# Kernel optimization log

Hardware: AMD Instinct MI355X
Metric: run time of the kernel (lower is better)

Reference implementation:

```python
import jax, jax.numpy as jnp
import numpy as np

# --- CQT configuration derived from the layer's __init__ defaults ---
SR = 44100
N_OCTAVES = 7
BINS_PER_SEMITONE = 3
BPO = BINS_PER_SEMITONE * 12            # 36 bins per octave
N_BINS = BPO * N_OCTAVES                # 252 bins
HOP = (int(SR * 11 / 1000.0) // 4) * 4  # 485 -> 484 (hop - hop % 4)
FMIN = 32.70319566257483                # librosa default fmin = C1
Q = 1.0 / (2.0 ** (1.0 / BPO) - 1.0)    # constant-Q factor, filter_scale=1

_FREQS = FMIN * 2.0 ** (np.arange(N_BINS) / BPO)   # [252] center freqs
_LENGTHS = Q * SR / _FREQS                         # per-bin window lengths
MAX_LEN = int(np.ceil(_LENGTHS[0]))                # longest kernel (lowest bin)
CENTER = MAX_LEN // 2
SIG_LEN = 220500                                   # 5 s of audio
N_FRAMES = 1 + SIG_LEN // HOP                      # 456 (centered framing)


def _cqt_kernels():
    """Complex CQT kernel bank, returned as (real, imag) of shape [N_BINS, MAX_LEN].
    Each bin uses a Hann window of its own constant-Q length, centered in MAX_LEN,
    modulated at its center frequency; L1-normalized window and 1/sqrt(L) scaling
    (matching librosa's norm=1 filters with scale=True)."""
    t = jnp.arange(MAX_LEN, dtype=jnp.float32) - CENTER          # centered time axis
    freqs = jnp.asarray(_FREQS, dtype=jnp.float32)[:, None]      # [252, 1]
    L = jnp.asarray(_LENGTHS, dtype=jnp.float32)[:, None]        # [252, 1]
    two_pi = 2.0 * np.pi
    # Hann window of length L_i centered at t=0, zero outside |t| < L_i/2
    win = jnp.where(jnp.abs(t)[None, :] < L / 2,
                    0.5 * (1.0 + jnp.cos(two_pi * t[None, :] / L)),
                    0.0)
    ang = two_pi * freqs * t[None, :] / SR
    norm = win.sum(axis=-1, keepdims=True) * jnp.sqrt(L)
    kr = win * jnp.cos(ang) / norm
    ki = win * jnp.sin(ang) / norm
    return kr, ki


def setup_inputs() -> dict:
    key = jax.random.key(0)
    signal = jax.random.normal(key, (SIG_LEN,), dtype=jnp.float32)
    return {"signal": signal}


def reference(signal) -> jnp.ndarray:
    kr, ki = _cqt_kernels()                                      # [252, MAX_LEN] each
    padded = jnp.pad(signal, (CENTER, CENTER))                   # center=True framing
    idx = (jnp.arange(N_FRAMES)[:, None] * HOP
           + jnp.arange(MAX_LEN)[None, :])                       # [456, MAX_LEN]
    frames = padded[idx]                                         # [456, MAX_LEN]
    cr = frames @ kr.T                                           # [456, 252] real part
    ci = frames @ ki.T                                           # [456, 252] imag part
    mag = jnp.sqrt(cr * cr + ci * ci)                            # |CQT|
    return mag.T                                                 # [252, 456] = (n_bins, n_frames)
```

## Files before the change

kernel.cpp:

```cpp
#include <hip/hip_runtime.h>
#include <hip/hip_bf16.h>
#include <math.h>

#define NBINS    252
#define NFRAMES  456
#define HOPSZ    484
#define SIGLEN   220500
#define PADOFF   34688
#define XBF_ELEMS 317440
#define SRD      44100.0
#define FMIND    32.70319566257483
#define TWO_PI_D 6.283185307179586476925287
#define MAXCH    288
#define SC       32
#define CHUNK_BYTES (SC*2048)
#define CHUNK_ELEMS (SC*1024)

typedef unsigned short ushort_t;
typedef __attribute__((ext_vector_type(8))) short bf16x8;
typedef __attribute__((ext_vector_type(4))) float f32x4;

struct ChunkTab { int2 e[MAXCH]; };

__global__ __launch_bounds__(256) void pad_bf16(const float* __restrict__ sig,
                                                ushort_t* __restrict__ xbf) {
  int i = blockIdx.x * 256 + threadIdx.x;
  if (i < XBF_ELEMS) {
    int s = i - PADOFF;
    float v = (s >= 0 && s < SIGLEN) ? sig[s] : 0.0f;
    __hip_bfloat16 h = __float2bfloat16(v);
    xbf[i] = *reinterpret_cast<ushort_t*>(&h);
  }
}

__global__ __launch_bounds__(256) void norm_kernel(float* __restrict__ nrm) {
  int b = blockIdx.x * 256 + threadIdx.x;
  if (b >= NBINS) return;
  const double PI = 3.14159265358979323846;
  double freq = FMIND * exp2((double)b / 36.0);
  double Q = 1.0 / (exp2(1.0 / 36.0) - 1.0);
  double L = Q * SRD / freq;
  int T = (int)(L * 0.5);
  double N = (double)(2 * T + 1);
  double win_sum = 0.5 * N - 0.5 * (sin(PI * (N - L) / L) / sin(PI / L));
  nrm[b] = (float)(1.0 / (win_sum * sqrt(L)));
}

__global__ __launch_bounds__(256) void gen_bank(ushort_t* __restrict__ bank, ChunkTab tab) {
  int c = blockIdx.y;
  int e = blockIdx.x * 256 + threadIdx.x;
  int ks = e >> 7;
  int rem = e & 127;
  int frag = (rem >> 6) & 1;
  int lane = rem & 63;
  int bl = lane & 15, kb = lane >> 4;
  int g = tab.e[c].x, jadj = tab.e[c].y;
  int b = g * 16 + bl;
  int t0 = jadj + ks * 32 + kb * 8;

  ushort_t res[8];
#pragma unroll
  for (int j = 0; j < 8; ++j) res[j] = 0;

  if (b < NBINS) {
    double freq = FMIND * exp2((double)b / 36.0);
    double fos = freq / SRD;
    double Q = 1.0 / (exp2(1.0 / 36.0) - 1.0);
    double L = Q * SRD / freq;
    int T = (int)(L * 0.5);
    if (t0 + 7 >= -T && t0 <= T) {
      double rv = fos * (double)t0; rv -= floor(rv);
      float ang0 = (float)(rv * TWO_PI_D);
      float dang = (float)(fos * TWO_PI_D);
      float invL = (float)(1.0 / L);
#pragma unroll
      for (int j = 0; j < 8; ++j) {
        int tt = t0 + j;
        if (tt >= -T && tt <= T) {
          float win = 0.5f + 0.5f * __cosf(6.2831853f * ((float)tt * invL));
          float s, cc;
          __sincosf(ang0 + (float)j * dang, &s, &cc);
          float val = win * (frag ? s : cc);
          __hip_bfloat16 h = __float2bfloat16(val);
          res[j] = *reinterpret_cast<ushort_t*>(&h);
        }
      }
    }
  }
  union { ushort_t u[8]; uint4 v; } pk;
#pragma unroll
  for (int j = 0; j < 8; ++j) pk.u[j] = res[j];
  *reinterpret_cast<uint4*>(bank + (size_t)c * CHUNK_ELEMS + ks * 1024 + frag * 512 + lane * 8) = pk.v;
}

__global__ __launch_bounds__(256) void zero_accum(float* __restrict__ acc) {
  acc[blockIdx.x * 256 + threadIdx.x] = 0.0f;
}

__global__ __launch_bounds__(256) void cqt_mfma(const ushort_t* __restrict__ xbf,
                                                const ushort_t* __restrict__ bank,
                                                float* __restrict__ accum,
                                                ChunkTab tab) {
  const int tid = threadIdx.x;
  const int lane = tid & 63;
  const int w = tid >> 6;
  const int c = blockIdx.y;
  const int g = tab.e[c].x, jadj = tab.e[c].y;
  const int bl = lane & 15, kb = lane >> 4;
  const int fbase = blockIdx.x * 128 + w * 32;

  const ushort_t* pA0 = xbf + (PADOFF + (fbase + bl) * HOPSZ + jadj + kb * 8);
  const ushort_t* pA1 = pA0 + 16 * HOPSZ;
  const ushort_t* pB  = bank + (size_t)c * CHUNK_ELEMS + lane * 8;

  f32x4 ar0 = {0.f, 0.f, 0.f, 0.f};
  f32x4 ai0 = ar0, ar1 = ar0, ai1 = ar0;

#pragma unroll 4
  for (int ks = 0; ks < SC; ++ks) {
    union { uint2 q[2]; bf16x8 v; } a0, a1;
    a0.q[0] = *reinterpret_cast<const uint2*>(pA0 + ks * 32);
    a0.q[1] = *reinterpret_cast<const uint2*>(pA0 + ks * 32 + 4);
    a1.q[0] = *reinterpret_cast<const uint2*>(pA1 + ks * 32);
    a1.q[1] = *reinterpret_cast<const uint2*>(pA1 + ks * 32 + 4);
    union { uint4 q; bf16x8 v; } bk, bi;
    bk.q = *reinterpret_cast<const uint4*>(pB + ks * 1024);
    bi.q = *reinterpret_cast<const uint4*>(pB + ks * 1024 + 512);
    ar0 = __builtin_amdgcn_mfma_f32_16x16x32_bf16(a0.v, bk.v, ar0, 0, 0, 0);
    ai0 = __builtin_amdgcn_mfma_f32_16x16x32_bf16(a0.v, bi.v, ai0, 0, 0, 0);
    ar1 = __builtin_amdgcn_mfma_f32_16x16x32_bf16(a1.v, bk.v, ar1, 0, 0, 0);
    ai1 = __builtin_amdgcn_mfma_f32_16x16x32_bf16(a1.v, bi.v, ai1, 0, 0, 0);
  }

  float* ap = accum + ((size_t)(g * 512 + fbase) * 16 + bl) * 2;
  const int row = kb * 4;
#pragma unroll
  for (int r = 0; r < 4; ++r) {
    atomicAdd(ap + (size_t)(row + r) * 32,            ar0[r]);
    atomicAdd(ap + (size_t)(row + r) * 32 + 1,        ai0[r]);
    atomicAdd(ap + (size_t)(row + r + 16) * 32,       ar1[r]);
    atomicAdd(ap + (size_t)(row + r + 16) * 32 + 1,   ai1[r]);
  }
}

__global__ __launch_bounds__(256) void fin_kernel(const float* __restrict__ accum,
                                                  const float* __restrict__ nrm,
                                                  float* __restrict__ out) {
  int id = blockIdx.x * 256 + threadIdx.x;
  if (id >= NBINS * NFRAMES) return;
  int b = id / NFRAMES;
  int f = id - b * NFRAMES;
  int g = b >> 4, bl = b & 15;
  size_t ai = ((size_t)(g * 512 + f) * 16 + bl) * 2;
  float cr = accum[ai], ci = accum[ai + 1];
  out[id] = nrm[b] * sqrtf(cr * cr + ci * ci);
}

extern "C" void kernel_launch(void* const* d_in, const int* in_sizes, int n_in,
                              void* d_out, int out_size, void* d_ws, size_t ws_size,
                              hipStream_t stream) {
  const float* sig = (const float*)d_in[0];
  float* out = (float*)d_out;
  char* ws = (char*)d_ws;

  ushort_t* xbf  = (ushort_t*)ws;
  ushort_t* bank = (ushort_t*)(ws + 634880);
  float* accum   = (float*)(ws + 634880 + (size_t)MAXCH * CHUNK_BYTES);
  float* nrm     = (float*)(ws + 634880 + (size_t)MAXCH * CHUNK_BYTES + 1048576);

  ChunkTab tab;
  int nch = 0;
  const double Q = 1.0 / (exp2(1.0 / 36.0) - 1.0);
  for (int gq = 0; gq < 16; ++gq) {
    double freq = FMIND * exp2((double)(16 * gq) / 36.0);
    double L = Q * SRD / freq;
    int T = (int)(L * 0.5);
    int r = (4 - (T & 3)) & 3;
    int tstart = -(T + r);
    int ntaps = 2 * T + 1 + r;
    int nsteps = (ntaps + 31) / 32;
    for (int ks0 = 0; ks0 < nsteps && nch < MAXCH; ks0 += SC) {
      tab.e[nch].x = gq;
      tab.e[nch].y = tstart + ks0 * 32;
      ++nch;
    }
  }
  for (int i = nch; i < MAXCH; ++i) { tab.e[i].x = 0; tab.e[i].y = 0; }

  pad_bf16<<<(XBF_ELEMS + 255) / 256, 256, 0, stream>>>(sig, xbf);
  norm_kernel<<<1, 256, 0, stream>>>(nrm);
  gen_bank<<<dim3(16, nch), 256, 0, stream>>>(bank, tab);
  zero_accum<<<1024, 256, 0, stream>>>(accum);
  cqt_mfma<<<dim3(4, nch), 256, 0, stream>>>(xbf, bank, accum, tab);
  fin_kernel<<<(NBINS * NFRAMES + 255) / 256, 256, 0, stream>>>(accum, nrm, out);
}
```

Baseline: 126.7 us.

## Replace atomic accumulation with per-segment partials reduced in finalize

Removes the zero_accum kernel and the float atomicAdds by having each MFMA block write its own partial sums for a segment of up to two chunks, and fin_kernel sums those partials per bin group. It also merges the norm computation into the padding kernel, which cuts two launches. Grouping two chunks per block halves the number of MFMA blocks and lengthens each block's K loop, which lowers parallelism across the GPU in exchange for fewer writes and launches.

```diff
diff --git a/kernel.cpp b/kernel.cpp
--- a/kernel.cpp
+++ b/kernel.cpp
@@ -12,6 +12,8 @@
 #define FMIND    32.70319566257483
 #define TWO_PI_D 6.283185307179586476925287
 #define MAXCH    288
+#define MAXSEG   144
+#define SEG      2
 #define SC       32
 #define CHUNK_BYTES (SC*2048)
 #define CHUNK_ELEMS (SC*1024)
@@ -21,9 +23,12 @@
 typedef __attribute__((ext_vector_type(4))) float f32x4;
 
 struct ChunkTab { int2 e[MAXCH]; };
-
-__global__ __launch_bounds__(256) void pad_bf16(const float* __restrict__ sig,
-                                                ushort_t* __restrict__ xbf) {
+struct SegTab   { int4 e[MAXSEG]; };
+struct GTab     { int2 e[16]; };
+
+__global__ __launch_bounds__(256) void setup_kernel(const float* __restrict__ sig,
+                                                    ushort_t* __restrict__ xbf,
+                                                    float* __restrict__ nrm) {
   int i = blockIdx.x * 256 + threadIdx.x;
   if (i < XBF_ELEMS) {
     int s = i - PADOFF;
@@ -31,19 +36,16 @@
     __hip_bfloat16 h = __float2bfloat16(v);
     xbf[i] = *reinterpret_cast<ushort_t*>(&h);
   }
-}
-
-__global__ __launch_bounds__(256) void norm_kernel(float* __restrict__ nrm) {
-  int b = blockIdx.x * 256 + threadIdx.x;
-  if (b >= NBINS) return;
-  const double PI = 3.14159265358979323846;
-  double freq = FMIND * exp2((double)b / 36.0);
-  double Q = 1.0 / (exp2(1.0 / 36.0) - 1.0);
-  double L = Q * SRD / freq;
-  int T = (int)(L * 0.5);
-  double N = (double)(2 * T + 1);
-  double win_sum = 0.5 * N - 0.5 * (sin(PI * (N - L) / L) / sin(PI / L));
-  nrm[b] = (float)(1.0 / (win_sum * sqrt(L)));
+  if (blockIdx.x == 0 && i < NBINS) {
+    const double PI = 3.14159265358979323846;
+    double freq = FMIND * exp2((double)i / 36.0);
+    double Q = 1.0 / (exp2(1.0 / 36.0) - 1.0);
+    double L = Q * SRD / freq;
+    int T = (int)(L * 0.5);
+    double N = (double)(2 * T + 1);
+    double win_sum = 0.5 * N - 0.5 * (sin(PI * (N - L) / L) / sin(PI / L));
+    nrm[i] = (float)(1.0 / (win_sum * sqrt(L)));
+  }
 }
 
 __global__ __launch_bounds__(256) void gen_bank(ushort_t* __restrict__ bank, ChunkTab tab) {
@@ -93,66 +95,66 @@
   *reinterpret_cast<uint4*>(bank + (size_t)c * CHUNK_ELEMS + ks * 1024 + frag * 512 + lane * 8) = pk.v;
 }
 
-__global__ __launch_bounds__(256) void zero_accum(float* __restrict__ acc) {
-  acc[blockIdx.x * 256 + threadIdx.x] = 0.0f;
-}
-
 __global__ __launch_bounds__(256) void cqt_mfma(const ushort_t* __restrict__ xbf,
                                                 const ushort_t* __restrict__ bank,
-                                                float* __restrict__ accum,
-                                                ChunkTab tab) {
+                                                float2* __restrict__ partial,
+                                                SegTab tab) {
   const int tid = threadIdx.x;
   const int lane = tid & 63;
   const int w = tid >> 6;
-  const int c = blockIdx.y;
-  const int g = tab.e[c].x, jadj = tab.e[c].y;
+  const int s = blockIdx.y;
+  const int c0 = tab.e[s].y;
+  const int nks = tab.e[s].z * SC;
+  const int jadj = tab.e[s].w;
   const int bl = lane & 15, kb = lane >> 4;
   const int fbase = blockIdx.x * 128 + w * 32;
 
   const ushort_t* pA0 = xbf + (PADOFF + (fbase + bl) * HOPSZ + jadj + kb * 8);
   const ushort_t* pA1 = pA0 + 16 * HOPSZ;
-  const ushort_t* pB  = bank + (size_t)c * CHUNK_ELEMS + lane * 8;
+  const ushort_t* pB  = bank + (size_t)c0 * CHUNK_ELEMS + lane * 8;
 
   f32x4 ar0 = {0.f, 0.f, 0.f, 0.f};
   f32x4 ai0 = ar0, ar1 = ar0, ai1 = ar0;
 
-#pragma unroll 4
-  for (int ks = 0; ks < SC; ++ks) {
+#pragma unroll 8
+  for (int ks = 0; ks < nks; ++ks) {
     union { uint2 q[2]; bf16x8 v; } a0, a1;
     a0.q[0] = *reinterpret_cast<const uint2*>(pA0 + ks * 32);
     a0.q[1] = *reinterpret_cast<const uint2*>(pA0 + ks * 32 + 4);
     a1.q[0] = *reinterpret_cast<const uint2*>(pA1 + ks * 32);
     a1.q[1] = *reinterpret_cast<const uint2*>(pA1 + ks * 32 + 4);
     union { uint4 q; bf16x8 v; } bk, bi;
-    bk.q = *reinterpret_cast<const uint4*>(pB + ks * 1024);
-    bi.q = *reinterpret_cast<const uint4*>(pB + ks * 1024 + 512);
+    bk.q = *reinterpret_cast<const uint4*>(pB + (size_t)ks * 1024);
+    bi.q = *reinterpret_cast<const uint4*>(pB + (size_t)ks * 1024 + 512);
     ar0 = __builtin_amdgcn_mfma_f32_16x16x32_bf16(a0.v, bk.v, ar0, 0, 0, 0);
     ai0 = __builtin_amdgcn_mfma_f32_16x16x32_bf16(a0.v, bi.v, ai0, 0, 0, 0);
     ar1 = __builtin_amdgcn_mfma_f32_16x16x32_bf16(a1.v, bk.v, ar1, 0, 0, 0);
     ai1 = __builtin_amdgcn_mfma_f32_16x16x32_bf16(a1.v, bi.v, ai1, 0, 0, 0);
   }
 
-  float* ap = accum + ((size_t)(g * 512 + fbase) * 16 + bl) * 2;
+  float2* pp = partial + ((size_t)s * 512 + fbase) * 16 + bl;
   const int row = kb * 4;
 #pragma unroll
   for (int r = 0; r < 4; ++r) {
-    atomicAdd(ap + (size_t)(row + r) * 32,            ar0[r]);
-    atomicAdd(ap + (size_t)(row + r) * 32 + 1,        ai0[r]);
-    atomicAdd(ap + (size_t)(row + r + 16) * 32,       ar1[r]);
-    atomicAdd(ap + (size_t)(row + r + 16) * 32 + 1,   ai1[r]);
-  }
-}
-
-__global__ __launch_bounds__(256) void fin_kernel(const float* __restrict__ accum,
+    pp[(size_t)(row + r) * 16]        = make_float2(ar0[r], ai0[r]);
+    pp[(size_t)(row + r + 16) * 16]   = make_float2(ar1[r], ai1[r]);
+  }
+}
+
+__global__ __launch_bounds__(256) void fin_kernel(const float2* __restrict__ partial,
                                                   const float* __restrict__ nrm,
-                                                  float* __restrict__ out) {
+                                                  float* __restrict__ out, GTab gt) {
   int id = blockIdx.x * 256 + threadIdx.x;
   if (id >= NBINS * NFRAMES) return;
   int b = id / NFRAMES;
   int f = id - b * NFRAMES;
   int g = b >> 4, bl = b & 15;
-  size_t ai = ((size_t)(g * 512 + f) * 16 + bl) * 2;
-  float cr = accum[ai], ci = accum[ai + 1];
+  int s0 = gt.e[g].x, sn = gt.e[g].y;
+  float cr = 0.f, ci = 0.f;
+  for (int s = s0; s < s0 + sn; ++s) {
+    float2 v = partial[((size_t)s * 512 + f) * 16 + bl];
+    cr += v.x; ci += v.y;
+  }
   out[id] = nrm[b] * sqrtf(cr * cr + ci * ci);
 }
 
@@ -163,13 +165,8 @@
   float* out = (float*)d_out;
   char* ws = (char*)d_ws;
 
-  ushort_t* xbf  = (ushort_t*)ws;
-  ushort_t* bank = (ushort_t*)(ws + 634880);
-  float* accum   = (float*)(ws + 634880 + (size_t)MAXCH * CHUNK_BYTES);
-  float* nrm     = (float*)(ws + 634880 + (size_t)MAXCH * CHUNK_BYTES + 1048576);
-
-  ChunkTab tab;
-  int nch = 0;
+  ChunkTab ctab; SegTab stab; GTab gtab;
+  int nch = 0, nseg = 0;
   const double Q = 1.0 / (exp2(1.0 / 36.0) - 1.0);
   for (int gq = 0; gq < 16; ++gq) {
     double freq = FMIND * exp2((double)(16 * gq) / 36.0);
@@ -179,18 +176,35 @@
     int tstart = -(T + r);
     int ntaps = 2 * T + 1 + r;
     int nsteps = (ntaps + 31) / 32;
-    for (int ks0 = 0; ks0 < nsteps && nch < MAXCH; ks0 += SC) {
-      tab.e[nch].x = gq;
-      tab.e[nch].y = tstart + ks0 * 32;
-      ++nch;
+    int chunks = (nsteps + SC - 1) / SC;
+    int base = nch;
+    for (int k = 0; k < chunks; ++k) {
+      ctab.e[nch].x = gq; ctab.e[nch].y = tstart + k * SC * 32; ++nch;
     }
-  }
-  for (int i = nch; i < MAXCH; ++i) { tab.e[i].x = 0; tab.e[i].y = 0; }
-
-  pad_bf16<<<(XBF_ELEMS + 255) / 256, 256, 0, stream>>>(sig, xbf);
-  norm_kernel<<<1, 256, 0, stream>>>(nrm);
-  gen_bank<<<dim3(16, nch), 256, 0, stream>>>(bank, tab);
-  zero_accum<<<1024, 256, 0, stream>>>(accum);
-  cqt_mfma<<<dim3(4, nch), 256, 0, stream>>>(xbf, bank, accum, tab);
-  fin_kernel<<<(NBINS * NFRAMES + 255) / 256, 256, 0, stream>>>(accum, nrm, out);
-}
+    gtab.e[gq].x = nseg;
+    for (int cs = 0; cs < chunks; cs += SEG) {
+      int nc = (chunks - cs) < SEG ? (chunks - cs) : SEG;
+      stab.e[nseg].x = gq;
+      stab.e[nseg].y = base + cs;
+      stab.e[nseg].z = nc;
+      stab.e[nseg].w = tstart + cs * SC * 32;
+      ++nseg;
+    }
+    gtab.e[gq].y = nseg - gtab.e[gq].x;
+  }
+  for (int i = nch; i < MAXCH; ++i)  { ctab.e[i].x = 0; ctab.e[i].y = 0; }
+  for (int i = nseg; i < MAXSEG; ++i){ stab.e[i].x = 0; stab.e[i].y = 0; stab.e[i].z = 1; stab.e[i].w = 0; }
+
+  ushort_t* xbf  = (ushort_t*)ws;
+  size_t off_bank = (size_t)XBF_ELEMS * 2;
+  ushort_t* bank = (ushort_t*)(ws + off_bank);
+  size_t off_part = off_bank + (size_t)nch * CHUNK_BYTES;
+  float2* partial = (float2*)(ws + off_part);
+  size_t off_nrm = off_part + (size_t)nseg * 512 * 16 * sizeof(float2);
+  float* nrm = (float*)(ws + off_nrm);
+
+  setup_kernel<<<(XBF_ELEMS + 255) / 256, 256, 0, stream>>>(sig, xbf, nrm);
+  gen_bank<<<dim3(16, nch), 256, 0, stream>>>(bank, ctab);
+  cqt_mfma<<<dim3(4, nseg), 256, 0, stream>>>(xbf, bank, partial, stab);
+  fin_kernel<<<(NBINS * NFRAMES + 255) / 256, 256, 0, stream>>>(partial, nrm, out, gtab);
+}
```

Result: no change. 127.5 us (+0.6%).

## Fuse kernel-bank generation into MFMA kernel via LDS and replace atomics with partials

Applied to the files above, without the earlier changes.

Each block now computes its own bf16 CQT kernel chunk in shared memory, replacing the separate gen_bank pass that wrote the bank to global memory. Each block covers 256 frames with 8 waves. Float atomics into a zeroed accumulator are replaced by per-chunk partial stores that fin_kernel sums, which also removes the zero_accum launch. The cost is recomputing trig per block (two frame tiles per chunk) and a serial reduction loop in the finalize kernel.

```diff
diff --git a/kernel.cpp b/kernel.cpp
--- a/kernel.cpp
+++ b/kernel.cpp
@@ -10,17 +10,20 @@
 #define XBF_ELEMS 317440
 #define SRD      44100.0
 #define FMIND    32.70319566257483
-#define TWO_PI_D 6.283185307179586476925287
-#define MAXCH    288
+#define MAXCH    264
 #define SC       32
-#define CHUNK_BYTES (SC*2048)
-#define CHUNK_ELEMS (SC*1024)
 
 typedef unsigned short ushort_t;
 typedef __attribute__((ext_vector_type(8))) short bf16x8;
 typedef __attribute__((ext_vector_type(4))) float f32x4;
 
 struct ChunkTab { int2 e[MAXCH]; };
+struct GTab     { int2 e[16]; };
+
+__device__ __forceinline__ ushort_t f2bf(float x) {
+  __hip_bfloat16 h = __float2bfloat16(x);
+  return *reinterpret_cast<ushort_t*>(&h);
+}
 
 __global__ __launch_bounds__(256) void pad_bf16(const float* __restrict__ sig,
                                                 ushort_t* __restrict__ xbf) {
@@ -28,95 +31,78 @@
   if (i < XBF_ELEMS) {
     int s = i - PADOFF;
     float v = (s >= 0 && s < SIGLEN) ? sig[s] : 0.0f;
-    __hip_bfloat16 h = __float2bfloat16(v);
-    xbf[i] = *reinterpret_cast<ushort_t*>(&h);
+    xbf[i] = f2bf(v);
   }
 }
 
-__global__ __launch_bounds__(256) void norm_kernel(float* __restrict__ nrm) {
-  int b = blockIdx.x * 256 + threadIdx.x;
-  if (b >= NBINS) return;
-  const double PI = 3.14159265358979323846;
-  double freq = FMIND * exp2((double)b / 36.0);
-  double Q = 1.0 / (exp2(1.0 / 36.0) - 1.0);
-  double L = Q * SRD / freq;
-  int T = (int)(L * 0.5);
-  double N = (double)(2 * T + 1);
-  double win_sum = 0.5 * N - 0.5 * (sin(PI * (N - L) / L) / sin(PI / L));
-  nrm[b] = (float)(1.0 / (win_sum * sqrt(L)));
-}
-
-__global__ __launch_bounds__(256) void gen_bank(ushort_t* __restrict__ bank, ChunkTab tab) {
-  int c = blockIdx.y;
-  int e = blockIdx.x * 256 + threadIdx.x;
-  int ks = e >> 7;
-  int rem = e & 127;
-  int frag = (rem >> 6) & 1;
-  int lane = rem & 63;
-  int bl = lane & 15, kb = lane >> 4;
-  int g = tab.e[c].x, jadj = tab.e[c].y;
-  int b = g * 16 + bl;
-  int t0 = jadj + ks * 32 + kb * 8;
-
-  ushort_t res[8];
-#pragma unroll
-  for (int j = 0; j < 8; ++j) res[j] = 0;
-
+__global__ void prep_kernel(float4* __restrict__ binc, float* __restrict__ nrm) {
+  int b = threadIdx.x;
+  if (b >= 256) return;
   if (b < NBINS) {
+    const double PI = 3.14159265358979323846;
     double freq = FMIND * exp2((double)b / 36.0);
     double fos = freq / SRD;
     double Q = 1.0 / (exp2(1.0 / 36.0) - 1.0);
     double L = Q * SRD / freq;
     int T = (int)(L * 0.5);
-    if (t0 + 7 >= -T && t0 <= T) {
-      double rv = fos * (double)t0; rv -= floor(rv);
-      float ang0 = (float)(rv * TWO_PI_D);
-      float dang = (float)(fos * TWO_PI_D);
-      float invL = (float)(1.0 / L);
+    double N = (double)(2 * T + 1);
+    double win_sum = 0.5 * N - 0.5 * (sin(PI * (N - L) / L) / sin(PI / L));
+    binc[b] = make_float4((float)fos, (float)(1.0 / L), (float)T, 0.0f);
+    nrm[b] = (float)(1.0 / (win_sum * sqrt(L)));
+  } else {
+    binc[b] = make_float4(0.0f, 0.0f, -1.0f, 0.0f);
+  }
+}
+
+__global__ __launch_bounds__(512) void cqt_fused(const ushort_t* __restrict__ xbf,
+                                                 const float4* __restrict__ binc,
+                                                 float2* __restrict__ partial,
+                                                 ChunkTab tab) {
+  __shared__ ushort_t blds[SC * 1024];
+
+  const int tid  = threadIdx.x;
+  const int lane = tid & 63;
+  const int bl   = lane & 15, kb = lane >> 4;
+  const int c    = blockIdx.y;
+  const int st   = blockIdx.x;
+  const int g    = tab.e[c].x, jadj = tab.e[c].y;
+
+  {
+    const float4 bc = binc[g * 16 + bl];
+    const float fos = bc.x, invL = bc.y, Tf = bc.z;
+    const int ksub = tid >> 6;
+#pragma unroll
+    for (int kq = 0; kq < 4; ++kq) {
+      const int ks = ksub + kq * 8;
+      const int t0 = jadj + ks * 32 + kb * 8;
+      union { ushort_t u[8]; uint4 v; } pr, pi;
 #pragma unroll
       for (int j = 0; j < 8; ++j) {
-        int tt = t0 + j;
-        if (tt >= -T && tt <= T) {
-          float win = 0.5f + 0.5f * __cosf(6.2831853f * ((float)tt * invL));
-          float s, cc;
-          __sincosf(ang0 + (float)j * dang, &s, &cc);
-          float val = win * (frag ? s : cc);
-          __hip_bfloat16 h = __float2bfloat16(val);
-          res[j] = *reinterpret_cast<ushort_t*>(&h);
+        const float tt = (float)(t0 + j);
+        float kr = 0.0f, ki = 0.0f;
+        if (fabsf(tt) <= Tf) {
+          float w = 0.5f + 0.5f * __cosf(6.2831853f * (tt * invL));
+          float r = fos * tt; r -= rintf(r);
+          float s, cc; __sincosf(6.2831853f * r, &s, &cc);
+          kr = w * cc; ki = w * s;
         }
+        pr.u[j] = f2bf(kr); pi.u[j] = f2bf(ki);
       }
+      *reinterpret_cast<uint4*>(&blds[ks * 1024 + lane * 8])       = pr.v;
+      *reinterpret_cast<uint4*>(&blds[ks * 1024 + 512 + lane * 8]) = pi.v;
     }
   }
-  union { ushort_t u[8]; uint4 v; } pk;
-#pragma unroll
-  for (int j = 0; j < 8; ++j) pk.u[j] = res[j];
-  *reinterpret_cast<uint4*>(bank + (size_t)c * CHUNK_ELEMS + ks * 1024 + frag * 512 + lane * 8) = pk.v;
-}
+  __syncthreads();
 
-__global__ __launch_bounds__(256) void zero_accum(float* __restrict__ acc) {
-  acc[blockIdx.x * 256 + threadIdx.x] = 0.0f;
-}
-
-__global__ __launch_bounds__(256) void cqt_mfma(const ushort_t* __restrict__ xbf,
-                                                const ushort_t* __restrict__ bank,
-                                                float* __restrict__ accum,
-                                                ChunkTab tab) {
-  const int tid = threadIdx.x;
-  const int lane = tid & 63;
   const int w = tid >> 6;
-  const int c = blockIdx.y;
-  const int g = tab.e[c].x, jadj = tab.e[c].y;
-  const int bl = lane & 15, kb = lane >> 4;
-  const int fbase = blockIdx.x * 128 + w * 32;
-
-  const ushort_t* pA0 = xbf + (PADOFF + (fbase + bl) * HOPSZ + jadj + kb * 8);
+  const int fbase = st * 256 + w * 32;
+  const ushort_t* pA0 = xbf + PADOFF + (fbase + bl) * HOPSZ + jadj + kb * 8;
   const ushort_t* pA1 = pA0 + 16 * HOPSZ;
-  const ushort_t* pB  = bank + (size_t)c * CHUNK_ELEMS + lane * 8;
 
   f32x4 ar0 = {0.f, 0.f, 0.f, 0.f};
   f32x4 ai0 = ar0, ar1 = ar0, ai1 = ar0;
 
-#pragma unroll 4
+#pragma unroll 8
   for (int ks = 0; ks < SC; ++ks) {
     union { uint2 q[2]; bf16x8 v; } a0, a1;
     a0.q[0] = *reinterpret_cast<const uint2*>(pA0 + ks * 32);
@@ -124,35 +110,38 @@
     a1.q[0] = *reinterpret_cast<const uint2*>(pA1 + ks * 32);
     a1.q[1] = *reinterpret_cast<const uint2*>(pA1 + ks * 32 + 4);
     union { uint4 q; bf16x8 v; } bk, bi;
-    bk.q = *reinterpret_cast<const uint4*>(pB + ks * 1024);
-    bi.q = *reinterpret_cast<const uint4*>(pB + ks * 1024 + 512);
+    bk.q = *reinterpret_cast<const uint4*>(&blds[ks * 1024 + lane * 8]);
+    bi.q = *reinterpret_cast<const uint4*>(&blds[ks * 1024 + 512 + lane * 8]);
     ar0 = __builtin_amdgcn_mfma_f32_16x16x32_bf16(a0.v, bk.v, ar0, 0, 0, 0);
     ai0 = __builtin_amdgcn_mfma_f32_16x16x32_bf16(a0.v, bi.v, ai0, 0, 0, 0);
     ar1 = __builtin_amdgcn_mfma_f32_16x16x32_bf16(a1.v, bk.v, ar1, 0, 0, 0);
     ai1 = __builtin_amdgcn_mfma_f32_16x16x32_bf16(a1.v, bi.v, ai1, 0, 0, 0);
   }
 
-  float* ap = accum + ((size_t)(g * 512 + fbase) * 16 + bl) * 2;
+  float2* pp = partial + ((size_t)(c * 2 + st) * 256 + w * 32) * 16 + bl;
   const int row = kb * 4;
 #pragma unroll
   for (int r = 0; r < 4; ++r) {
-    atomicAdd(ap + (size_t)(row + r) * 32,            ar0[r]);
-    atomicAdd(ap + (size_t)(row + r) * 32 + 1,        ai0[r]);
-    atomicAdd(ap + (size_t)(row + r + 16) * 32,       ar1[r]);
-    atomicAdd(ap + (size_t)(row + r + 16) * 32 + 1,   ai1[r]);
+    pp[(size_t)(row + r) * 16]      = make_float2(ar0[r], ai0[r]);
+    pp[(size_t)(row + r + 16) * 16] = make_float2(ar1[r], ai1[r]);
   }
 }
 
-__global__ __launch_bounds__(256) void fin_kernel(const float* __restrict__ accum,
+__global__ __launch_bounds__(256) void fin_kernel(const float2* __restrict__ partial,
                                                   const float* __restrict__ nrm,
-                                                  float* __restrict__ out) {
+                                                  float* __restrict__ out, GTab gt) {
   int id = blockIdx.x * 256 + threadIdx.x;
   if (id >= NBINS * NFRAMES) return;
   int b = id / NFRAMES;
   int f = id - b * NFRAMES;
   int g = b >> 4, bl = b & 15;
-  size_t ai = ((size_t)(g * 512 + f) * 16 + bl) * 2;
-  float cr = accum[ai], ci = accum[ai + 1];
+  int st = f >> 8, fl = f & 255;
+  int c0 = gt.e[g].x, nc = gt.e[g].y;
+  float cr = 0.f, ci = 0.f;
+  for (int c = c0; c < c0 + nc; ++c) {
+    float2 v = partial[((size_t)(c * 2 + st) * 256 + fl) * 16 + bl];
+    cr += v.x; ci += v.y;
+  }
   out[id] = nrm[b] * sqrtf(cr * cr + ci * ci);
 }
 
@@ -163,12 +152,7 @@
   float* out = (float*)d_out;
   char* ws = (char*)d_ws;
 
-  ushort_t* xbf  = (ushort_t*)ws;
-  ushort_t* bank = (ushort_t*)(ws + 634880);
-  float* accum   = (float*)(ws + 634880 + (size_t)MAXCH * CHUNK_BYTES);
-  float* nrm     = (float*)(ws + 634880 + (size_t)MAXCH * CHUNK_BYTES + 1048576);
-
-  ChunkTab tab;
+  ChunkTab ctab; GTab gtab;
   int nch = 0;
   const double Q = 1.0 / (exp2(1.0 / 36.0) - 1.0);
   for (int gq = 0; gq < 16; ++gq) {
@@ -178,19 +162,22 @@
     int r = (4 - (T & 3)) & 3;
     int tstart = -(T + r);
     int ntaps = 2 * T + 1 + r;
-    int nsteps = (ntaps + 31) / 32;
-    for (int ks0 = 0; ks0 < nsteps && nch < MAXCH; ks0 += SC) {
-      tab.e[nch].x = gq;
-      tab.e[nch].y = tstart + ks0 * 32;
-      ++nch;
+    int chunks = (ntaps + SC * 32 - 1) / (SC * 32);
+    gtab.e[gq].x = nch; gtab.e[gq].y = chunks;
+    for (int k = 0; k < chunks; ++k) {
+      ctab.e[nch].x = gq; ctab.e[nch].y = tstart + k * SC * 32; ++nch;
     }
   }
-  for (int i = nch; i < MAXCH; ++i) { tab.e[i].x = 0; tab.e[i].y = 0; }
+  for (int i = nch; i < MAXCH; ++i) { ctab.e[i].x = 0; ctab.e[i].y = 0; }
+
+  ushort_t* xbf = (ushort_t*)ws;
+  size_t off = (size_t)XBF_ELEMS * 2;
+  float4* binc = (float4*)(ws + off);  off += 256 * sizeof(float4);
+  float* nrm   = (float*)(ws + off);   off += 256 * sizeof(float);
+  float2* partial = (float2*)(ws + ((off + 255) & ~(size_t)255));
 
   pad_bf16<<<(XBF_ELEMS + 255) / 256, 256, 0, stream>>>(sig, xbf);
-  norm_kernel<<<1, 256, 0, stream>>>(nrm);
-  gen_bank<<<dim3(16, nch), 256, 0, stream>>>(bank, tab);
-  zero_accum<<<1024, 256, 0, stream>>>(accum);
-  cqt_mfma<<<dim3(4, nch), 256, 0, stream>>>(xbf, bank, accum, tab);
-  fin_kernel<<<(NBINS * NFRAMES + 255) / 256, 256, 0, stream>>>(accum, nrm, out);
+  prep_kernel<<<1, 256, 0, stream>>>(binc, nrm);
+  cqt_fused<<<dim3(2, nch), 512, 0, stream>>>(xbf, binc, partial, ctab);
+  fin_kernel<<<(NBINS * NFRAMES + 255) / 256, 256, 0, stream>>>(partial, nrm, out, gtab);
 }
```

After: 121.5 us. 1.04x faster.
